# Kernel tuning notes

Hardware: AMD Instinct MI355X
Metric: run time of the kernel (lower is better)

Reference implementation:

```python
import jax, jax.numpy as jnp
import numpy as np

V, E, H, T, B, A = 100000, 300, 256, 128, 64, 8
FH, NC = 256, 2
G = 2 * H  # gcn_input_dim = hidden_size * 2


def setup_inputs() -> dict:
    key = jax.random.key(0)
    ks = jax.random.split(key, 28)
    def n(k, shape, scale=0.05):
        return jax.random.normal(k, shape, dtype=jnp.float32) * scale
    return {
        "sentence": jax.random.randint(ks[0], (B, T), 0, V),
        "aspect": jax.random.randint(ks[1], (B, A), 0, V),
        "pos_class": jax.random.randint(ks[2], (B, T), 0, 18),
        "dep_tags": jax.random.randint(ks[3], (B, T), 0, 40),
        "text_len": jax.random.randint(ks[4], (B,), 1, T + 1),
        "aspect_len": jax.random.randint(ks[5], (B,), 1, A + 1),
        "dep_rels": jax.random.randint(ks[6], (B, T), 0, 40),
        "dep_heads": jax.random.randint(ks[7], (B, T), 0, T),
        "aspect_position": jax.random.randint(ks[8], (B, T), 0, 2),
        "dep_dirs": jax.random.randint(ks[9], (B, T), 0, 3),
        # frozen GloVe table
        "glove_emb": jax.random.normal(ks[10], (V, E), dtype=jnp.float32),
        # BiLSTM (1 layer): PyTorch layout, gates ordered i,f,g,o
        "w_ih_f": n(ks[11], (4 * H, E)), "w_hh_f": n(ks[12], (4 * H, H)),
        "b_ih_f": n(ks[13], (4 * H,)), "b_hh_f": n(ks[14], (4 * H,)),
        "w_ih_b": n(ks[15], (4 * H, E)), "w_hh_b": n(ks[16], (4 * H, H)),
        "b_ih_b": n(ks[17], (4 * H,)), "b_hh_b": n(ks[18], (4 * H,)),
        # 'gcn' attention branch: self.gat = nn.Linear(G, G)
        "gat_w": n(ks[19], (G, G)), "gat_b": n(ks[20], (G,)),
        # fcs MLP (num_mlps = 2)
        "fc1_w": n(ks[21], (FH, G)), "fc1_b": n(ks[22], (FH,)),
        "fc2_w": n(ks[23], (FH, FH)), "fc2_b": n(ks[24], (FH,)),
        "fcf_w": n(ks[25], (NC, FH)), "fcf_b": n(ks[26], (NC,)),
    }


def _lstm_dir(x, w_ih, w_hh, b_ih, b_hh, reverse):
    """One direction of a PyTorch-style LSTM. x: (B, T, E) -> (B, T, H)."""
    Bn = x.shape[0]
    Hh = w_hh.shape[1]
    xs = jnp.swapaxes(x, 0, 1)  # (T, B, E)
    if reverse:
        xs = xs[::-1]
    def step(carry, xt):
        h, c = carry
        g = xt @ w_ih.T + b_ih + h @ w_hh.T + b_hh  # (B, 4H)
        i, f, gg, o = jnp.split(g, 4, axis=-1)
        c = jax.nn.sigmoid(f) * c + jax.nn.sigmoid(i) * jnp.tanh(gg)
        h = jax.nn.sigmoid(o) * jnp.tanh(c)
        return (h, c), h
    init = (jnp.zeros((Bn, Hh), x.dtype), jnp.zeros((Bn, Hh), x.dtype))
    _, hs = jax.lax.scan(step, init, xs)
    if reverse:
        hs = hs[::-1]
    return jnp.swapaxes(hs, 0, 1)


def _bilstm(x, w_ih_f, w_hh_f, b_ih_f, b_hh_f, w_ih_b, w_hh_b, b_ih_b, b_hh_b):
    fwd = _lstm_dir(x, w_ih_f, w_hh_f, b_ih_f, b_hh_f, reverse=False)
    bwd = _lstm_dir(x, w_ih_b, w_hh_b, b_ih_b, b_hh_b, reverse=True)
    return jnp.concatenate([fwd, bwd], axis=-1)  # (B, T, 2H)


def reference(sentence, aspect, pos_class, dep_tags, text_len, aspect_len,
              dep_rels, dep_heads, aspect_position, dep_dirs,
              glove_emb, w_ih_f, w_hh_f, b_ih_f, b_hh_f,
              w_ih_b, w_hh_b, b_ih_b, b_hh_b,
              gat_w, gat_b, fc1_w, fc1_b, fc2_w, fc2_b, fcf_w, fcf_b):
    # fmask: per-token validity mask derived from text_len (inputs_to_deprel_adj)
    fmask = (jnp.arange(T)[None, :] < text_len[:, None]).astype(jnp.float32)  # (B, T)
    # embedding lookup (dropout is identity in eval mode)
    feature = glove_emb[sentence]  # (B, T, E)
    # BiLSTM over the sentence. (aspect branch is dead code in the 'gcn' path:
    # aspect_feature is computed but never used, so we omit it.)
    feature = _bilstm(feature, w_ih_f, w_hh_f, b_ih_f, b_hh_f,
                      w_ih_b, w_hh_b, b_ih_b, b_hh_b)  # (B, T, 2H)
    # 'gcn' branch: linear, mask, sum over tokens, relu
    gat_out = feature @ gat_w.T + gat_b           # (B, T, 2H)
    gat_out = gat_out * fmask[:, :, None]
    gat_out = jax.nn.relu(jnp.sum(gat_out, axis=1))  # (B, 2H)
    # fcs MLP + final classifier
    x = jax.nn.relu(gat_out @ fc1_w.T + fc1_b)
    x = jax.nn.relu(x @ fc2_w.T + fc2_b)
    logit = x @ fcf_w.T + fcf_b                    # (B, NC)
    return logit
```

## Files before the change

kernel.cpp:

```cpp
#include <hip/hip_runtime.h>
#include <hip/hip_bf16.h>
#include <math.h>

#define B_  64
#define T_  128
#define E_  300
#define H_  256
#define G4  1024
#define N2  2048
#define GG  512
#define FH_ 256
#define NC_ 2
#define KP  320

typedef __attribute__((ext_vector_type(8))) short short8;
typedef __attribute__((ext_vector_type(4))) float f32x4;
typedef unsigned short ushort_t;
typedef unsigned long long u64;

static __device__ __forceinline__ ushort_t bf16bits(float x) {
    __hip_bfloat16 b = __float2bfloat16(x);
    return __builtin_bit_cast(ushort_t, b);
}
static __device__ __forceinline__ float bf16lo(unsigned v) {
    return __builtin_bit_cast(float, v << 16);
}
static __device__ __forceinline__ float bf16hi(unsigned v) {
    return __builtin_bit_cast(float, v & 0xffff0000u);
}

#define OFF_CNT   131072
#define OFF_BIAS  262144
#define OFF_WIH   1048576
#define OFF_XEMB  2621440
#define OFF_XPROJ 8388608
#define OFF_S     41943040
#define INIT_U32  ((131072 + 256) / 4)

__global__ void k_init(unsigned* __restrict__ p) {
    int i = blockIdx.x * 256 + threadIdx.x;
    if (i < INIT_U32) p[i] = 0;
}

__global__ __launch_bounds__(256) void k_emb(
    const int*   __restrict__ sentence,
    const float* __restrict__ glove,
    ushort_t*    __restrict__ xemb) {
    const int idx = blockIdx.x * 256 + threadIdx.x;
    const int m  = idx / 80;
    const int c4 = (idx % 80) * 4;
    const float* row = glove + (size_t)sentence[m] * E_;
    ushort_t o[4];
    #pragma unroll
    for (int j = 0; j < 4; ++j) {
        const int k = c4 + j;
        o[j] = (k < E_) ? bf16bits(row[k]) : (ushort_t)0;
    }
    uint2 pk;
    pk.x = (unsigned)o[0] | ((unsigned)o[1] << 16);
    pk.y = (unsigned)o[2] | ((unsigned)o[3] << 16);
    *(uint2*)(xemb + (size_t)m * KP + c4) = pk;
}

__global__ __launch_bounds__(256) void k_wih(
    const float* __restrict__ w_ih_f,
    const float* __restrict__ w_ih_b,
    ushort_t*    __restrict__ wihshuf) {
    const int p = blockIdx.x * 256 + threadIdx.x;
    const int ntile = p / 640;
    const int r     = p % 640;
    const int ks    = r / 64;
    const int lane  = r % 64;
    const int n  = ntile * 16 + (lane & 15);
    const int k0 = ks * 32 + ((lane >> 4) << 3);
    const float* src = (n < G4) ? (w_ih_f + (size_t)n * E_)
                                : (w_ih_b + (size_t)(n - G4) * E_);
    ushort_t o[8];
    #pragma unroll
    for (int j = 0; j < 8; ++j) {
        const int k = k0 + j;
        o[j] = (k < E_) ? bf16bits(src[k]) : (ushort_t)0;
    }
    uint4 pk;
    pk.x = (unsigned)o[0] | ((unsigned)o[1] << 16);
    pk.y = (unsigned)o[2] | ((unsigned)o[3] << 16);
    pk.z = (unsigned)o[4] | ((unsigned)o[5] << 16);
    pk.w = (unsigned)o[6] | ((unsigned)o[7] << 16);
    *(uint4*)(wihshuf + (size_t)p * 8) = pk;
}

__global__ void k_bias(const float* __restrict__ b_ih_f, const float* __restrict__ b_hh_f,
                       const float* __restrict__ b_ih_b, const float* __restrict__ b_hh_b,
                       float* __restrict__ bias2) {
    const int n = blockIdx.x * 256 + threadIdx.x;
    bias2[n] = (n < G4) ? (b_ih_f[n] + b_hh_f[n])
                        : (b_ih_b[n - G4] + b_hh_b[n - G4]);
}

__global__ __launch_bounds__(256) void k_xproj_mfma(
    const ushort_t* __restrict__ xemb,
    const ushort_t* __restrict__ wihshuf,
    const float*    __restrict__ bias2,
    ushort_t*       __restrict__ xprojb) {
    const int tid = threadIdx.x;
    const int wave = tid >> 6, lane = tid & 63;
    const int quad = lane >> 4, l15 = lane & 15;
    const int m0 = blockIdx.x * 64 + wave * 16;
    const ushort_t* ap = xemb + (size_t)(m0 + l15) * KP;
    const ushort_t* wp = wihshuf + (size_t)blockIdx.y * 8 * 5120 + lane * 8;

    f32x4 acc[8] = {};
    #pragma unroll
    for (int ks = 0; ks < 10; ++ks) {
        short8 af = *(const short8*)(ap + ks * 32 + quad * 8);
        #pragma unroll
        for (int j = 0; j < 8; ++j) {
            short8 bf = *(const short8*)(wp + (size_t)(j * 10 + ks) * 512);
            acc[j] = __builtin_amdgcn_mfma_f32_16x16x32_bf16(af, bf, acc[j], 0, 0, 0);
        }
    }
    #pragma unroll
    for (int j = 0; j < 8; ++j) {
        const int n = blockIdx.y * 128 + j * 16 + l15;
        const float bias = bias2[n];
        #pragma unroll
        for (int r = 0; r < 4; ++r) {
            const int m = m0 + quad * 4 + r;
            xprojb[(size_t)m * N2 + n] = bf16bits(acc[j][r] + bias);
        }
    }
}

__global__ __launch_bounds__(256, 1) void k_lstm_sync(
    const ushort_t* __restrict__ xprojb,
    const float*    __restrict__ w_hh_f,
    const float*    __restrict__ w_hh_b,
    const int*      __restrict__ text_len,
    ushort_t*       __restrict__ hbuf,
    int*            __restrict__ cnt,
    float*          __restrict__ S)
{
    __shared__ float gLDS[4 * 16 * 33];

    const int tid   = threadIdx.x;
    const int g     = blockIdx.x & 7;
    const int slice = blockIdx.x >> 3;
    const int d     = g & 1;
    const int b0    = (g >> 1) * 16;
    const int j0    = slice * 32;
    const int wave  = tid >> 6, lane = tid & 63;
    const int quad  = lane >> 4, l15 = lane & 15;

    const float* whh = d ? w_hh_b : w_hh_f;
    int* cnt_g = cnt + g * 8;

    short8 wfrag[2][8];
    #pragma unroll
    for (int u = 0; u < 2; ++u) {
        const int n = wave * 256 + j0 + u * 16 + l15;
        #pragma unroll
        for (int ks = 0; ks < 8; ++ks) {
            const float* p = whh + (size_t)n * 256 + ks * 32 + quad * 8;
            float4 lo = *(const float4*)p;
            float4 hi = *(const float4*)(p + 4);
            short8 f;
            f[0] = (short)bf16bits(lo.x); f[1] = (short)bf16bits(lo.y);
            f[2] = (short)bf16bits(lo.z); f[3] = (short)bf16bits(lo.w);
            f[4] = (short)bf16bits(hi.x); f[5] = (short)bf16bits(hi.y);
            f[6] = (short)bf16bits(hi.z); f[7] = (short)bf16bits(hi.w);
            wfrag[u][ks] = f;
        }
    }

    const int mb = tid >> 4;
    const int c0 = (tid & 15) * 2;
    const int lenm = text_len[b0 + mb];
    float cst0 = 0.f, cst1 = 0.f, s0 = 0.f, s1 = 0.f;

    for (int t = 0; t < T_; ++t) {
        const int tt = d ? (T_ - 1 - t) : t;
        const ushort_t* xp = xprojb +
            ((size_t)(b0 + mb) * T_ + tt) * N2 + d * G4 + j0;
        const unsigned vi = *(const unsigned*)(xp + c0);
        const unsigned vf = *(const unsigned*)(xp + 256 + c0);
        const unsigned vg = *(const unsigned*)(xp + 512 + c0);
        const unsigned vo = *(const unsigned*)(xp + 768 + c0);

        if (t > 0 && wave == 0 && lane < 8) {
            while (__hip_atomic_load(&cnt_g[lane], __ATOMIC_RELAXED,
                                     __HIP_MEMORY_SCOPE_AGENT) < t) {}
        }
        __syncthreads();

        const u64* hin64 = (const u64*)(hbuf + (size_t)(t & 1) * 32768 +
                                        g * 4096 + l15 * 256);
        short8 af[8];
        #pragma unroll
        for (int ks = 0; ks < 8; ++ks) {
            union { u64 u[2]; short8 v; } cv;
            cv.u[0] = __hip_atomic_load(hin64 + ks * 8 + quad * 2,
                                        __ATOMIC_RELAXED, __HIP_MEMORY_SCOPE_AGENT);
            cv.u[1] = __hip_atomic_load(hin64 + ks * 8 + quad * 2 + 1,
                                        __ATOMIC_RELAXED, __HIP_MEMORY_SCOPE_AGENT);
            af[ks] = cv.v;
        }
        f32x4 acc[2] = {};
        #pragma unroll
        for (int ks = 0; ks < 8; ++ks) {
            acc[0] = __builtin_amdgcn_mfma_f32_16x16x32_bf16(
                af[ks], wfrag[0][ks], acc[0], 0, 0, 0);
            acc[1] = __builtin_amdgcn_mfma_f32_16x16x32_bf16(
                af[ks], wfrag[1][ks], acc[1], 0, 0, 0);
        }
        #pragma unroll
        for (int u = 0; u < 2; ++u)
            #pragma unroll
            for (int r = 0; r < 4; ++r)
                gLDS[wave * 528 + (quad * 4 + r) * 33 + u * 16 + l15] = acc[u][r];
        __syncthreads();

        const int gb = mb * 33 + c0;
        const float gi0 = gLDS[gb],        gi1 = gLDS[gb + 1];
        const float gf0 = gLDS[528 + gb],  gf1 = gLDS[528 + gb + 1];
        const float gg0 = gLDS[1056 + gb], gg1 = gLDS[1056 + gb + 1];
        const float go0 = gLDS[1584 + gb], go1 = gLDS[1584 + gb + 1];
        const float i0 = 1.f / (1.f + __expf(-(bf16lo(vi) + gi0)));
        const float i1 = 1.f / (1.f + __expf(-(bf16hi(vi) + gi1)));
        const float f0 = 1.f / (1.f + __expf(-(bf16lo(vf) + gf0)));
        const float f1 = 1.f / (1.f + __expf(-(bf16hi(vf) + gf1)));
        const float gc0 = tanhf(bf16lo(vg) + gg0);
        const float gc1 = tanhf(bf16hi(vg) + gg1);
        const float o0 = 1.f / (1.f + __expf(-(bf16lo(vo) + go0)));
        const float o1 = 1.f / (1.f + __expf(-(bf16hi(vo) + go1)));
        cst0 = f0 * cst0 + i0 * gc0;
        cst1 = f1 * cst1 + i1 * gc1;
        const float h0 = o0 * tanhf(cst0);
        const float h1 = o1 * tanhf(cst1);
        if (tt < lenm) { s0 += h0; s1 += h1; }

        unsigned* hout = (unsigned*)(hbuf + (size_t)((t + 1) & 1) * 32768 +
                                     g * 4096 + mb * 256 + j0 + c0);
        const unsigned hp = (unsigned)bf16bits(h0) | ((unsigned)bf16bits(h1) << 16);
        __hip_atomic_store(hout, hp, __ATOMIC_RELAXED, __HIP_MEMORY_SCOPE_AGENT);
        __syncthreads();
        if (tid == 0)
            __hip_atomic_store(&cnt_g[slice], t + 1, __ATOMIC_RELAXED,
                               __HIP_MEMORY_SCOPE_AGENT);
    }

    float2 sv; sv.x = s0; sv.y = s1;
    *(float2*)(S + (size_t)(b0 + mb) * GG + d * H_ + j0 + c0) = sv;
}

__global__ __launch_bounds__(256) void k_head(
    const float* __restrict__ S,
    const int*   __restrict__ text_len,
    const float* __restrict__ gat_w, const float* __restrict__ gat_b,
    const float* __restrict__ fc1_w, const float* __restrict__ fc1_b,
    const float* __restrict__ fc2_w, const float* __restrict__ fc2_b,
    const float* __restrict__ fcf_w, const float* __restrict__ fcf_b,
    float* __restrict__ out)
{
    __shared__ float sb[GG];
    __shared__ float x1[GG];
    __shared__ float x2[FH_];
    __shared__ float x3[FH_];
    const int b = blockIdx.x, tid = threadIdx.x;
    sb[tid]       = S[(size_t)b * GG + tid];
    sb[tid + 256] = S[(size_t)b * GG + tid + 256];
    __syncthreads();
    const float lenf = (float)text_len[b];
    #pragma unroll
    for (int r = 0; r < 2; ++r) {
        const int n = tid + r * 256;
        float acc = gat_b[n] * lenf;
        const float* w = gat_w + (size_t)n * GG;
        for (int k = 0; k < GG; ++k) acc += sb[k] * w[k];
        x1[n] = fmaxf(acc, 0.f);
    }
    __syncthreads();
    {
        float acc = fc1_b[tid];
        const float* w = fc1_w + (size_t)tid * GG;
        for (int k = 0; k < GG; ++k) acc += x1[k] * w[k];
        x2[tid] = fmaxf(acc, 0.f);
    }
    __syncthreads();
    {
        float acc = fc2_b[tid];
        const float* w = fc2_w + (size_t)tid * FH_;
        for (int k = 0; k < FH_; ++k) acc += x2[k] * w[k];
        x3[tid] = fmaxf(acc, 0.f);
    }
    __syncthreads();
    if (tid < NC_) {
        float acc = fcf_b[tid];
        const float* w = fcf_w + (size_t)tid * FH_;
        for (int k = 0; k < FH_; ++k) acc += x3[k] * w[k];
        out[b * NC_ + tid] = acc;
    }
}

extern "C" void kernel_launch(void* const* d_in, const int* in_sizes, int n_in,
                              void* d_out, int out_size, void* d_ws, size_t ws_size,
                              hipStream_t stream) {
    const int*   sentence = (const int*)  d_in[0];
    const int*   text_len = (const int*)  d_in[4];
    const float* glove    = (const float*)d_in[10];
    const float* w_ih_f   = (const float*)d_in[11];
    const float* w_hh_f   = (const float*)d_in[12];
    const float* b_ih_f   = (const float*)d_in[13];
    const float* b_hh_f   = (const float*)d_in[14];
    const float* w_ih_b   = (const float*)d_in[15];
    const float* w_hh_b   = (const float*)d_in[16];
    const float* b_ih_b   = (const float*)d_in[17];
    const float* b_hh_b   = (const float*)d_in[18];
    const float* gat_w    = (const float*)d_in[19];
    const float* gat_b    = (const float*)d_in[20];
    const float* fc1_w    = (const float*)d_in[21];
    const float* fc1_b    = (const float*)d_in[22];
    const float* fc2_w    = (const float*)d_in[23];
    const float* fc2_b    = (const float*)d_in[24];
    const float* fcf_w    = (const float*)d_in[25];
    const float* fcf_b    = (const float*)d_in[26];
    float* out = (float*)d_out;

    char* ws = (char*)d_ws;
    ushort_t* hbuf    = (ushort_t*)ws;
    int*      cnt     = (int*)(ws + OFF_CNT);
    float*    bias2   = (float*)(ws + OFF_BIAS);
    ushort_t* wihshuf = (ushort_t*)(ws + OFF_WIH);
    ushort_t* xemb    = (ushort_t*)(ws + OFF_XEMB);
    ushort_t* xprojb  = (ushort_t*)(ws + OFF_XPROJ);
    float*    S       = (float*)(ws + OFF_S);

    k_init<<<(INIT_U32 + 255) / 256, 256, 0, stream>>>((unsigned*)d_ws);
    k_emb<<<2560, 256, 0, stream>>>(sentence, glove, xemb);
    k_wih<<<320, 256, 0, stream>>>(w_ih_f, w_ih_b, wihshuf);
    k_bias<<<8, 256, 0, stream>>>(b_ih_f, b_hh_f, b_ih_b, b_hh_b, bias2);
    dim3 gx(128, 16);
    k_xproj_mfma<<<gx, 256, 0, stream>>>(xemb, wihshuf, bias2, xprojb);
    k_lstm_sync<<<64, 256, 0, stream>>>(xprojb, w_hh_f, w_hh_b, text_len,
                                        hbuf, cnt, S);
    k_head<<<64, 256, 0, stream>>>(S, text_len, gat_w, gat_b,
                                   fc1_w, fc1_b, fc2_w, fc2_b,
                                   fcf_w, fcf_b, out);
}
```

Baseline: 789.9 us.

## Replace counter barrier with step-tagged h words and fuse prep kernels

Each hidden-state value is now published as a 64-bit word whose upper half holds the step index. Consumers spin on the data words themselves, staged through LDS by one wave, instead of on per-slice counters. This removes a syncthreads, a separate flag store and a dependent round trip from every recurrent step. The four setup kernels are merged into one launch, and the input projection writes its output through shared memory as coalesced 16-byte stores. The cost is doubled hbuf traffic, heavier polling reads, and reliance on stale tags in the unzeroed second slab never matching the expected step.

```diff
diff --git a/kernel.cpp b/kernel.cpp
--- a/kernel.cpp
+++ b/kernel.cpp
@@ -29,72 +29,70 @@
     return __builtin_bit_cast(float, v & 0xffff0000u);
 }
 
-#define OFF_CNT   131072
 #define OFF_BIAS  262144
-#define OFF_WIH   1048576
-#define OFF_XEMB  2621440
+#define OFF_WIH   524288
+#define OFF_XEMB  2097152
 #define OFF_XPROJ 8388608
 #define OFF_S     41943040
-#define INIT_U32  ((131072 + 256) / 4)
-
-__global__ void k_init(unsigned* __restrict__ p) {
-    int i = blockIdx.x * 256 + threadIdx.x;
-    if (i < INIT_U32) p[i] = 0;
-}
-
-__global__ __launch_bounds__(256) void k_emb(
+
+__global__ __launch_bounds__(256) void k_prep(
     const int*   __restrict__ sentence,
     const float* __restrict__ glove,
+    const float* __restrict__ w_ih_f,
+    const float* __restrict__ w_ih_b,
+    const float* __restrict__ b_ih_f, const float* __restrict__ b_hh_f,
+    const float* __restrict__ b_ih_b, const float* __restrict__ b_hh_b,
+    u64*         __restrict__ hbuf,
+    float*       __restrict__ bias2,
+    ushort_t*    __restrict__ wihshuf,
     ushort_t*    __restrict__ xemb) {
     const int idx = blockIdx.x * 256 + threadIdx.x;
-    const int m  = idx / 80;
-    const int c4 = (idx % 80) * 4;
-    const float* row = glove + (size_t)sentence[m] * E_;
-    ushort_t o[4];
-    #pragma unroll
-    for (int j = 0; j < 4; ++j) {
-        const int k = c4 + j;
-        o[j] = (k < E_) ? bf16bits(row[k]) : (ushort_t)0;
-    }
-    uint2 pk;
-    pk.x = (unsigned)o[0] | ((unsigned)o[1] << 16);
-    pk.y = (unsigned)o[2] | ((unsigned)o[3] << 16);
-    *(uint2*)(xemb + (size_t)m * KP + c4) = pk;
-}
-
-__global__ __launch_bounds__(256) void k_wih(
-    const float* __restrict__ w_ih_f,
-    const float* __restrict__ w_ih_b,
-    ushort_t*    __restrict__ wihshuf) {
-    const int p = blockIdx.x * 256 + threadIdx.x;
-    const int ntile = p / 640;
-    const int r     = p % 640;
-    const int ks    = r / 64;
-    const int lane  = r % 64;
-    const int n  = ntile * 16 + (lane & 15);
-    const int k0 = ks * 32 + ((lane >> 4) << 3);
-    const float* src = (n < G4) ? (w_ih_f + (size_t)n * E_)
-                                : (w_ih_b + (size_t)(n - G4) * E_);
-    ushort_t o[8];
-    #pragma unroll
-    for (int j = 0; j < 8; ++j) {
-        const int k = k0 + j;
-        o[j] = (k < E_) ? bf16bits(src[k]) : (ushort_t)0;
-    }
-    uint4 pk;
-    pk.x = (unsigned)o[0] | ((unsigned)o[1] << 16);
-    pk.y = (unsigned)o[2] | ((unsigned)o[3] << 16);
-    pk.z = (unsigned)o[4] | ((unsigned)o[5] << 16);
-    pk.w = (unsigned)o[6] | ((unsigned)o[7] << 16);
-    *(uint4*)(wihshuf + (size_t)p * 8) = pk;
-}
-
-__global__ void k_bias(const float* __restrict__ b_ih_f, const float* __restrict__ b_hh_f,
-                       const float* __restrict__ b_ih_b, const float* __restrict__ b_hh_b,
-                       float* __restrict__ bias2) {
-    const int n = blockIdx.x * 256 + threadIdx.x;
-    bias2[n] = (n < G4) ? (b_ih_f[n] + b_hh_f[n])
-                        : (b_ih_b[n - G4] + b_hh_b[n - G4]);
+
+    if (idx < 16384) hbuf[idx] = 0ull;
+
+    if (idx < N2) {
+        bias2[idx] = (idx < G4) ? (b_ih_f[idx] + b_hh_f[idx])
+                                : (b_ih_b[idx - G4] + b_hh_b[idx - G4]);
+    }
+
+    if (idx < 81920) {
+        const int ntile = idx / 640;
+        const int r     = idx % 640;
+        const int ks    = r / 64;
+        const int lane  = r % 64;
+        const int n  = ntile * 16 + (lane & 15);
+        const int k0 = ks * 32 + ((lane >> 4) << 3);
+        const float* src = (n < G4) ? (w_ih_f + (size_t)n * E_)
+                                    : (w_ih_b + (size_t)(n - G4) * E_);
+        ushort_t o[8];
+        #pragma unroll
+        for (int j = 0; j < 8; ++j) {
+            const int k = k0 + j;
+            o[j] = (k < E_) ? bf16bits(src[k]) : (ushort_t)0;
+        }
+        uint4 pk;
+        pk.x = (unsigned)o[0] | ((unsigned)o[1] << 16);
+        pk.y = (unsigned)o[2] | ((unsigned)o[3] << 16);
+        pk.z = (unsigned)o[4] | ((unsigned)o[5] << 16);
+        pk.w = (unsigned)o[6] | ((unsigned)o[7] << 16);
+        *(uint4*)(wihshuf + (size_t)idx * 8) = pk;
+    }
+
+    {
+        const int m  = idx / 80;
+        const int c4 = (idx % 80) * 4;
+        const float* row = glove + (size_t)sentence[m] * E_;
+        ushort_t o[4];
+        #pragma unroll
+        for (int j = 0; j < 4; ++j) {
+            const int k = c4 + j;
+            o[j] = (k < E_) ? bf16bits(row[k]) : (ushort_t)0;
+        }
+        uint2 pk;
+        pk.x = (unsigned)o[0] | ((unsigned)o[1] << 16);
+        pk.y = (unsigned)o[2] | ((unsigned)o[3] << 16);
+        *(uint2*)(xemb + (size_t)m * KP + c4) = pk;
+    }
 }
 
 __global__ __launch_bounds__(256) void k_xproj_mfma(
@@ -102,12 +100,13 @@
     const ushort_t* __restrict__ wihshuf,
     const float*    __restrict__ bias2,
     ushort_t*       __restrict__ xprojb) {
+    __shared__ ushort_t ct[4][16][136];
     const int tid = threadIdx.x;
     const int wave = tid >> 6, lane = tid & 63;
     const int quad = lane >> 4, l15 = lane & 15;
     const int m0 = blockIdx.x * 64 + wave * 16;
     const ushort_t* ap = xemb + (size_t)(m0 + l15) * KP;
-    const ushort_t* wp = wihshuf + (size_t)blockIdx.y * 8 * 5120 + lane * 8;
+    const ushort_t* wp = wihshuf + (size_t)blockIdx.y * 40960 + lane * 8;
 
     f32x4 acc[8] = {};
     #pragma unroll
@@ -121,13 +120,16 @@
     }
     #pragma unroll
     for (int j = 0; j < 8; ++j) {
-        const int n = blockIdx.y * 128 + j * 16 + l15;
-        const float bias = bias2[n];
-        #pragma unroll
-        for (int r = 0; r < 4; ++r) {
-            const int m = m0 + quad * 4 + r;
-            xprojb[(size_t)m * N2 + n] = bf16bits(acc[j][r] + bias);
-        }
+        const float bias = bias2[blockIdx.y * 128 + j * 16 + l15];
+        #pragma unroll
+        for (int r = 0; r < 4; ++r)
+            ct[wave][quad * 4 + r][j * 16 + l15] = bf16bits(acc[j][r] + bias);
+    }
+    #pragma unroll
+    for (int i = 0; i < 4; ++i) {
+        const int row = i * 4 + (lane >> 4);
+        uint4 v = *(const uint4*)&ct[wave][row][l15 * 8];
+        *(uint4*)(xprojb + (size_t)(m0 + row) * N2 + blockIdx.y * 128 + l15 * 8) = v;
     }
 }
 
@@ -136,11 +138,11 @@
     const float*    __restrict__ w_hh_f,
     const float*    __restrict__ w_hh_b,
     const int*      __restrict__ text_len,
-    ushort_t*       __restrict__ hbuf,
-    int*            __restrict__ cnt,
+    u64*            __restrict__ hbuf,
     float*          __restrict__ S)
 {
-    __shared__ float gLDS[4 * 16 * 33];
+    __shared__ ushort_t hl[16][264];
+    __shared__ float    gLDS[4 * 16 * 33];
 
     const int tid   = threadIdx.x;
     const int g     = blockIdx.x & 7;
@@ -152,7 +154,8 @@
     const int quad  = lane >> 4, l15 = lane & 15;
 
     const float* whh = d ? w_hh_b : w_hh_f;
-    int* cnt_g = cnt + g * 8;
+    u64* slab0 = hbuf + (size_t)g * 2048;
+    u64* slab1 = hbuf + 16384 + (size_t)g * 2048;
 
     short8 wfrag[2][8];
     #pragma unroll
@@ -173,6 +176,7 @@
     }
 
     const int mb = tid >> 4;
+    const int wi = mb * 128 + slice * 16 + (tid & 15);
     const int c0 = (tid & 15) * 2;
     const int lenm = text_len[b0 + mb];
     float cst0 = 0.f, cst1 = 0.f, s0 = 0.f, s1 = 0.f;
@@ -186,24 +190,36 @@
         const unsigned vg = *(const unsigned*)(xp + 512 + c0);
         const unsigned vo = *(const unsigned*)(xp + 768 + c0);
 
-        if (t > 0 && wave == 0 && lane < 8) {
-            while (__hip_atomic_load(&cnt_g[lane], __ATOMIC_RELAXED,
-                                     __HIP_MEMORY_SCOPE_AGENT) < t) {}
+        if (wave == 0) {
+            const u64* src = ((t & 1) ? slab1 : slab0) +
+                             (lane & 15) * 128 + (lane >> 4) * 32;
+            u64 v[32];
+            bool ok = false;
+            while (!ok) {
+                ok = true;
+                #pragma unroll
+                for (int i = 0; i < 32; ++i)
+                    v[i] = __hip_atomic_load(src + i, __ATOMIC_RELAXED,
+                                             __HIP_MEMORY_SCOPE_AGENT);
+                #pragma unroll
+                for (int i = 0; i < 32; ++i)
+                    ok = ok && ((unsigned)(v[i] >> 32) == (unsigned)t);
+            }
+            ushort_t* drow = &hl[lane & 15][(lane >> 4) * 64];
+            #pragma unroll
+            for (int i = 0; i < 16; ++i) {
+                uint2 pk;
+                pk.x = (unsigned)v[2 * i];
+                pk.y = (unsigned)v[2 * i + 1];
+                *(uint2*)(drow + i * 4) = pk;
+            }
         }
         __syncthreads();
 
-        const u64* hin64 = (const u64*)(hbuf + (size_t)(t & 1) * 32768 +
-                                        g * 4096 + l15 * 256);
         short8 af[8];
         #pragma unroll
-        for (int ks = 0; ks < 8; ++ks) {
-            union { u64 u[2]; short8 v; } cv;
-            cv.u[0] = __hip_atomic_load(hin64 + ks * 8 + quad * 2,
-                                        __ATOMIC_RELAXED, __HIP_MEMORY_SCOPE_AGENT);
-            cv.u[1] = __hip_atomic_load(hin64 + ks * 8 + quad * 2 + 1,
-                                        __ATOMIC_RELAXED, __HIP_MEMORY_SCOPE_AGENT);
-            af[ks] = cv.v;
-        }
+        for (int ks = 0; ks < 8; ++ks)
+            af[ks] = *(const short8*)&hl[l15][ks * 32 + quad * 8];
         f32x4 acc[2] = {};
         #pragma unroll
         for (int ks = 0; ks < 8; ++ks) {
@@ -238,14 +254,12 @@
         const float h1 = o1 * tanhf(cst1);
         if (tt < lenm) { s0 += h0; s1 += h1; }
 
-        unsigned* hout = (unsigned*)(hbuf + (size_t)((t + 1) & 1) * 32768 +
-                                     g * 4096 + mb * 256 + j0 + c0);
-        const unsigned hp = (unsigned)bf16bits(h0) | ((unsigned)bf16bits(h1) << 16);
-        __hip_atomic_store(hout, hp, __ATOMIC_RELAXED, __HIP_MEMORY_SCOPE_AGENT);
-        __syncthreads();
-        if (tid == 0)
-            __hip_atomic_store(&cnt_g[slice], t + 1, __ATOMIC_RELAXED,
-                               __HIP_MEMORY_SCOPE_AGENT);
+        const u64 word = ((u64)(unsigned)(t + 1) << 32) |
+                         (u64)((unsigned)bf16bits(h0) |
+                               ((unsigned)bf16bits(h1) << 16));
+        u64* dst = ((t & 1) ? slab0 : slab1) + wi;
+        __hip_atomic_store(dst, word, __ATOMIC_RELAXED,
+                           __HIP_MEMORY_SCOPE_AGENT);
     }
 
     float2 sv; sv.x = s0; sv.y = s1;
@@ -326,22 +340,20 @@
     float* out = (float*)d_out;
 
     char* ws = (char*)d_ws;
-    ushort_t* hbuf    = (ushort_t*)ws;
-    int*      cnt     = (int*)(ws + OFF_CNT);
+    u64*      hbuf    = (u64*)ws;
     float*    bias2   = (float*)(ws + OFF_BIAS);
     ushort_t* wihshuf = (ushort_t*)(ws + OFF_WIH);
     ushort_t* xemb    = (ushort_t*)(ws + OFF_XEMB);
     ushort_t* xprojb  = (ushort_t*)(ws + OFF_XPROJ);
     float*    S       = (float*)(ws + OFF_S);
 
-    k_init<<<(INIT_U32 + 255) / 256, 256, 0, stream>>>((unsigned*)d_ws);
-    k_emb<<<2560, 256, 0, stream>>>(sentence, glove, xemb);
-    k_wih<<<320, 256, 0, stream>>>(w_ih_f, w_ih_b, wihshuf);
-    k_bias<<<8, 256, 0, stream>>>(b_ih_f, b_hh_f, b_ih_b, b_hh_b, bias2);
+    k_prep<<<2560, 256, 0, stream>>>(sentence, glove, w_ih_f, w_ih_b,
+                                     b_ih_f, b_hh_f, b_ih_b, b_hh_b,
+                                     hbuf, bias2, wihshuf, xemb);
     dim3 gx(128, 16);
     k_xproj_mfma<<<gx, 256, 0, stream>>>(xemb, wihshuf, bias2, xprojb);
     k_lstm_sync<<<64, 256, 0, stream>>>(xprojb, w_hh_f, w_hh_b, text_len,
-                                        hbuf, cnt, S);
+                                        hbuf, S);
     k_head<<<64, 256, 0, stream>>>(S, text_len, gat_w, gat_b,
                                    fc1_w, fc1_b, fc2_w, fc2_b,
                                    fcf_w, fcf_b, out);
```

Result: faster. 746.1 us (-5.5%).
